# Kernel tuning notes

Measured on AMD Instinct MI355X. Metric: run time of the kernel, lower is better.

Reference implementation:

```python
import jax, jax.numpy as jnp
import numpy as np

B, N, D_IN, D_OUT = 2, 768, 64, 64
TEMP = 2.0
BN_EPS = 1e-5


def setup_inputs() -> dict:
    key = jax.random.key(0)
    ks = jax.random.split(key, 12)
    s_in = 1.0 / np.sqrt(D_IN)
    return {
        "x": jax.random.normal(ks[0], (B, N, D_IN), jnp.float32),
        # att_proj: Linear(in_dim, out_dim), stored as [in, out]
        "W_att": jax.random.uniform(ks[1], (D_IN, D_OUT), jnp.float32, -s_in, s_in),
        "b_att": jax.random.uniform(ks[2], (D_OUT,), jnp.float32, -s_in, s_in),
        # att_weight: [out_dim, 1] -> stored squeezed [out_dim]
        "a_w": jax.random.normal(ks[3], (D_OUT,), jnp.float32) * np.sqrt(2.0 / (D_OUT + 1)),
        "W_p": jax.random.uniform(ks[4], (D_IN, D_OUT), jnp.float32, -s_in, s_in),
        "b_p": jax.random.uniform(ks[5], (D_OUT,), jnp.float32, -s_in, s_in),
        "W_q": jax.random.uniform(ks[6], (D_IN, D_OUT), jnp.float32, -s_in, s_in),
        "b_q": jax.random.uniform(ks[7], (D_OUT,), jnp.float32, -s_in, s_in),
        # BatchNorm1d eval-mode params / running stats
        "gamma": jnp.ones((D_OUT,), jnp.float32),
        "beta": jnp.zeros((D_OUT,), jnp.float32),
        "r_mean": jax.random.normal(ks[8], (D_OUT,), jnp.float32) * 0.1,
        "r_var": jax.random.uniform(ks[9], (D_OUT,), jnp.float32, 0.5, 1.5),
    }


def reference(x, W_att, b_att, a_w, W_p, b_p, W_q, b_q, gamma, beta, r_mean, r_var):
    # pairwise node product: [B, N, N, D]
    pm = x[:, :, None, :] * x[:, None, :, :]
    # tanh(att_proj(pm)) @ att_weight -> scalar score per (i, j)
    h = jnp.tanh(jnp.einsum("bijd,do->bijo", pm, W_att) + b_att)
    scores = jnp.einsum("bijo,o->bij", h, a_w) / TEMP
    # softmax over dim=-2 of [B,N,N,1] == the j (second node) axis
    att = jax.nn.softmax(scores, axis=2)  # [B, N, N]
    # attention-weighted aggregation + skip projection
    agg = jnp.einsum("bij,bjd->bid", att, x)  # [B, N, D]
    y = agg @ W_p + b_p + x @ W_q + b_q  # [B, N, D_OUT]
    # BatchNorm1d (eval mode, running stats)
    y = (y - r_mean) * (gamma / jnp.sqrt(r_var + BN_EPS)) + beta
    return jax.nn.selu(y)
```

## Files before the change

kernel.cpp:

```cpp
#include <hip/hip_runtime.h>
#include <hip/hip_bf16.h>

constexpr int Bc = 2;
constexpr int Nc = 768;
constexpr int Dc = 64;

typedef __attribute__((ext_vector_type(8))) short short8;
typedef __attribute__((ext_vector_type(4))) short short4v;
typedef __attribute__((ext_vector_type(4))) float f32x4;

#define TWO_LOG2E 2.8853900817779268f

__device__ inline short fbf(float f) {
    __hip_bfloat16 h = __float2bfloat16(f);
    return *reinterpret_cast<short*>(&h);
}

__global__ __launch_bounds__(256)
void prep_kernel(const float* __restrict__ x, short* __restrict__ xb)
{
    const int idx = blockIdx.x * 256 + threadIdx.x;
    const float4 v = ((const float4*)x)[idx];
    short4v o;
    o[0] = fbf(v.x); o[1] = fbf(v.y); o[2] = fbf(v.z); o[3] = fbf(v.w);
    ((short4v*)xb)[idx] = o;
}

__global__ __launch_bounds__(256, 4)
void scores_kernel(const float* __restrict__ x,
                   const short* __restrict__ xbf,
                   const float* __restrict__ W_att,
                   const float* __restrict__ b_att,
                   const float* __restrict__ a_w,
                   float* __restrict__ sc)
{
    __shared__ short s_A[Dc * Dc];
    __shared__ float s_xi[Dc];

    const int blk = blockIdx.x;
    const int b   = blk & 1;
    const int i   = blk >> 1;
    const int tid  = threadIdx.x;
    const int lane = tid & 63;
    const int wid  = tid >> 6;

    const float* xb  = x   + (size_t)b * Nc * Dc;
    const short* xbb = xbf + (size_t)b * Nc * Dc;

    if (tid < Dc) s_xi[tid] = xb[i * Dc + tid];
    __syncthreads();

    {
        const int d0 = wid * 16;
        float m0[16];
#pragma unroll
        for (int dd = 0; dd < 16; ++dd)
            m0[dd] = s_xi[d0 + dd] * W_att[(d0 + dd) * Dc + lane];
#pragma unroll
        for (int c8 = 0; c8 < 2; ++c8) {
            short8 v;
#pragma unroll
            for (int e = 0; e < 8; ++e) v[e] = fbf(m0[c8 * 8 + e]);
            const int c    = wid * 2 + c8;
            const int phys = c ^ (lane & 7);
            *(short8*)(&s_A[lane * Dc + phys * 8]) = v;
        }
    }

    float tb2[16], aw[16];
#pragma unroll
    for (int mt = 0; mt < 4; ++mt)
#pragma unroll
        for (int r = 0; r < 4; ++r) {
            const int o = 16 * mt + 4 * (lane >> 4) + r;
            tb2[mt * 4 + r] = TWO_LOG2E * b_att[o];
            aw [mt * 4 + r] = a_w[o];
        }
    float sa = 0.f;
#pragma unroll
    for (int k = 0; k < 16; ++k) sa += aw[k];
    sa += __shfl_xor(sa, 16, 64);
    sa += __shfl_xor(sa, 32, 64);
    const float half_sum_aw = 0.5f * sa;
    __syncthreads();

    short8 afr[4][2];
#pragma unroll
    for (int mt = 0; mt < 4; ++mt)
#pragma unroll
        for (int kt = 0; kt < 2; ++kt) {
            const int o    = 16 * mt + (lane & 15);
            const int c    = (lane >> 4) + 4 * kt;
            const int phys = c ^ (o & 7);
            afr[mt][kt] = *(const short8*)(&s_A[o * Dc + phys * 8]);
        }

    float* srow = sc + ((size_t)b * Nc + i) * Nc;
    const int t0 = i >> 4;

    int t = t0 + wid;
    if (t < 48) {
        const short* p0 = xbb + (size_t)(16 * t + (lane & 15)) * Dc + (lane >> 4) * 8;
        short8 c0 = *(const short8*)p0;
        short8 c1 = *(const short8*)(p0 + 32);
        while (t < 48) {
            const int tn = t + 4;
            short8 n0, n1;
            if (tn < 48) {
                const short* p1 = xbb + (size_t)(16 * tn + (lane & 15)) * Dc + (lane >> 4) * 8;
                n0 = *(const short8*)p1;
                n1 = *(const short8*)(p1 + 32);
            }

            f32x4 ac[4];
#pragma unroll
            for (int mt = 0; mt < 4; ++mt) {
                ac[mt] = (f32x4){0.f, 0.f, 0.f, 0.f};
                ac[mt] = __builtin_amdgcn_mfma_f32_16x16x32_bf16(afr[mt][0], c0, ac[mt], 0, 0, 0);
                ac[mt] = __builtin_amdgcn_mfma_f32_16x16x32_bf16(afr[mt][1], c1, ac[mt], 0, 0, 0);
            }

            float p = 0.f;
#pragma unroll
            for (int mt = 0; mt < 4; ++mt)
#pragma unroll
                for (int r = 0; r < 4; ++r) {
                    const float m = fmaf(ac[mt][r], TWO_LOG2E, tb2[mt * 4 + r]);
                    const float e = __builtin_amdgcn_exp2f(m);
                    const float rc = __builtin_amdgcn_rcpf(e + 1.f);
                    p = fmaf(aw[mt * 4 + r], rc, p);
                }
            p += __shfl_xor(p, 16, 64);
            p += __shfl_xor(p, 32, 64);

            const int j = 16 * t + lane;
            if (lane < 16 && j >= i) srow[j] = half_sum_aw - p;
            c0 = n0; c1 = n1; t = tn;
        }
    }
}

__global__ __launch_bounds__(256, 4)
void finish_kernel(const float* __restrict__ x,
                   const float* __restrict__ sc,
                   const float* __restrict__ W_p,
                   const float* __restrict__ b_p,
                   const float* __restrict__ W_q,
                   const float* __restrict__ b_q,
                   const float* __restrict__ gamma,
                   const float* __restrict__ beta,
                   const float* __restrict__ r_mean,
                   const float* __restrict__ r_var,
                   float* __restrict__ out)
{
    __shared__ float s_score[Nc];
    __shared__ float s_xi[Dc];
    __shared__ float s_red[4][Dc];
    __shared__ float s_tmp[4];

    const int blk = blockIdx.x;
    const int b   = blk & 1;
    const int i   = blk >> 1;
    const int tid  = threadIdx.x;
    const int lane = tid & 63;
    const int wid  = tid >> 6;

    const float* xb = x + (size_t)b * Nc * Dc;
    if (tid < Dc) s_xi[tid] = xb[i * Dc + tid];

    const float* srow = sc + ((size_t)b * Nc + i) * Nc;
    for (int j = i + tid; j < Nc; j += 256) s_score[j] = srow[j];
    for (int j = tid; j < i; j += 256)      s_score[j] = sc[((size_t)b * Nc + j) * Nc + i];
    __syncthreads();

    float mx = -1e30f;
    for (int j = tid; j < Nc; j += 256) mx = fmaxf(mx, s_score[j]);
#pragma unroll
    for (int off = 32; off; off >>= 1)
        mx = fmaxf(mx, __shfl_xor(mx, off, 64));
    if (lane == 0) s_tmp[wid] = mx;
    __syncthreads();
    mx = fmaxf(fmaxf(s_tmp[0], s_tmp[1]), fmaxf(s_tmp[2], s_tmp[3]));
    __syncthreads();

    float sm = 0.f;
    for (int j = tid; j < Nc; j += 256) {
        const float e = __expf(s_score[j] - mx);
        s_score[j] = e;
        sm += e;
    }
#pragma unroll
    for (int off = 32; off; off >>= 1)
        sm += __shfl_xor(sm, off, 64);
    if (lane == 0) s_tmp[wid] = sm;
    __syncthreads();
    const float inv_sum = 1.f / (s_tmp[0] + s_tmp[1] + s_tmp[2] + s_tmp[3]);

    float aggp = 0.f;
    const int j0 = wid * (Nc / 4), j1 = j0 + Nc / 4;
    for (int j = j0; j < j1; ++j)
        aggp = fmaf(s_score[j], xb[j * Dc + lane], aggp);
    s_red[wid][lane] = aggp;
    __syncthreads();

    if (wid == 0)
        s_red[0][lane] = (s_red[0][lane] + s_red[1][lane] +
                          s_red[2][lane] + s_red[3][lane]) * inv_sum;
    __syncthreads();

    if (wid == 0) {
        float y = b_p[lane] + b_q[lane];
#pragma unroll 8
        for (int d = 0; d < Dc; ++d) {
            y = fmaf(s_red[0][d], W_p[d * Dc + lane], y);
            y = fmaf(s_xi[d],     W_q[d * Dc + lane], y);
        }
        const float inv_std = rsqrtf(r_var[lane] + 1e-5f);
        y = (y - r_mean[lane]) * (gamma[lane] * inv_std) + beta[lane];
        const float kScale = 1.0507009873554805f;
        const float kAlpha = 1.6732632423543772f;
        y = y > 0.f ? kScale * y : kScale * kAlpha * (__expf(y) - 1.f);
        out[((size_t)b * Nc + i) * Dc + lane] = y;
    }
}

__global__ __launch_bounds__(256, 4)
void mono_kernel(const float* __restrict__ x,
                 const float* __restrict__ W_att,
                 const float* __restrict__ b_att,
                 const float* __restrict__ a_w,
                 const float* __restrict__ W_p,
                 const float* __restrict__ b_p,
                 const float* __restrict__ W_q,
                 const float* __restrict__ b_q,
                 const float* __restrict__ gamma,
                 const float* __restrict__ beta,
                 const float* __restrict__ r_mean,
                 const float* __restrict__ r_var,
                 float* __restrict__ out)
{
    __shared__ short s_A[Dc * Dc];
    __shared__ float s_score[Nc];
    __shared__ float s_xi[Dc];
    __shared__ float s_red[4][Dc];
    __shared__ float s_tmp[4];

    const int bid = blockIdx.x;
    const int b   = bid / Nc;
    const int i   = bid - b * Nc;
    const int tid  = threadIdx.x;
    const int lane = tid & 63;
    const int wid  = tid >> 6;

    const float* xb = x + (size_t)b * Nc * Dc;
    if (tid < Dc) s_xi[tid] = xb[i * Dc + tid];
    __syncthreads();

    {
        const int d0 = wid * 16;
        float m0[16];
#pragma unroll
        for (int dd = 0; dd < 16; ++dd)
            m0[dd] = s_xi[d0 + dd] * W_att[(d0 + dd) * Dc + lane];
#pragma unroll
        for (int c8 = 0; c8 < 2; ++c8) {
            short8 v;
#pragma unroll
            for (int e = 0; e < 8; ++e) v[e] = fbf(m0[c8 * 8 + e]);
            const int c    = wid * 2 + c8;
            const int phys = c ^ (lane & 7);
            *(short8*)(&s_A[lane * Dc + phys * 8]) = v;
        }
    }

    float tb[16], aw[16];
#pragma unroll
    for (int mt = 0; mt < 4; ++mt)
#pragma unroll
        for (int r = 0; r < 4; ++r) {
            const int o = 16 * mt + 4 * (lane >> 4) + r;
            tb[mt * 4 + r] = 2.f * b_att[o];
            aw[mt * 4 + r] = a_w[o];
        }
    __syncthreads();

    short8 afr[4][2];
#pragma unroll
    for (int mt = 0; mt < 4; ++mt)
#pragma unroll
        for (int kt = 0; kt < 2; ++kt) {
            const int o    = 16 * mt + (lane & 15);
            const int c    = (lane >> 4) + 4 * kt;
            const int phys = c ^ (o & 7);
            afr[mt][kt] = *(const short8*)(&s_A[o * Dc + phys * 8]);
        }

    const int jbase = wid * 192;
    for (int t = 0; t < 12; ++t) {
        const int j0 = jbase + t * 16;
        const float* xr = xb + (size_t)(j0 + (lane & 15)) * Dc + (lane >> 4) * 8;
        const float4 v0 = *(const float4*)(xr);
        const float4 v1 = *(const float4*)(xr + 4);
        const float4 v2 = *(const float4*)(xr + 32);
        const float4 v3 = *(const float4*)(xr + 36);
        short8 bf0, bf1;
        bf0[0]=fbf(v0.x); bf0[1]=fbf(v0.y); bf0[2]=fbf(v0.z); bf0[3]=fbf(v0.w);
        bf0[4]=fbf(v1.x); bf0[5]=fbf(v1.y); bf0[6]=fbf(v1.z); bf0[7]=fbf(v1.w);
        bf1[0]=fbf(v2.x); bf1[1]=fbf(v2.y); bf1[2]=fbf(v2.z); bf1[3]=fbf(v2.w);
        bf1[4]=fbf(v3.x); bf1[5]=fbf(v3.y); bf1[6]=fbf(v3.z); bf1[7]=fbf(v3.w);

        f32x4 ac[4];
#pragma unroll
        for (int mt = 0; mt < 4; ++mt) {
            ac[mt] = (f32x4){0.f, 0.f, 0.f, 0.f};
            ac[mt] = __builtin_amdgcn_mfma_f32_16x16x32_bf16(afr[mt][0], bf0, ac[mt], 0, 0, 0);
            ac[mt] = __builtin_amdgcn_mfma_f32_16x16x32_bf16(afr[mt][1], bf1, ac[mt], 0, 0, 0);
        }

        float p = 0.f;
#pragma unroll
        for (int mt = 0; mt < 4; ++mt)
#pragma unroll
            for (int r = 0; r < 4; ++r) {
                const float e  = __expf(fmaf(ac[mt][r], 2.f, tb[mt * 4 + r]));
                const float th = 1.f - 2.f * __builtin_amdgcn_rcpf(e + 1.f);
                p = fmaf(th, aw[mt * 4 + r], p);
            }
        p += __shfl_xor(p, 16, 64);
        p += __shfl_xor(p, 32, 64);
        if (lane < 16) s_score[j0 + lane] = p * 0.5f;
    }
    __syncthreads();

    float mx = -1e30f;
    for (int j = tid; j < Nc; j += 256) mx = fmaxf(mx, s_score[j]);
#pragma unroll
    for (int off = 32; off; off >>= 1)
        mx = fmaxf(mx, __shfl_xor(mx, off, 64));
    if (lane == 0) s_tmp[wid] = mx;
    __syncthreads();
    mx = fmaxf(fmaxf(s_tmp[0], s_tmp[1]), fmaxf(s_tmp[2], s_tmp[3]));
    __syncthreads();

    float sm = 0.f;
    for (int j = tid; j < Nc; j += 256) {
        const float e = __expf(s_score[j] - mx);
        s_score[j] = e;
        sm += e;
    }
#pragma unroll
    for (int off = 32; off; off >>= 1)
        sm += __shfl_xor(sm, off, 64);
    if (lane == 0) s_tmp[wid] = sm;
    __syncthreads();
    const float inv_sum = 1.f / (s_tmp[0] + s_tmp[1] + s_tmp[2] + s_tmp[3]);

    float aggp = 0.f;
    const int j0 = wid * (Nc / 4), j1 = j0 + Nc / 4;
    for (int j = j0; j < j1; ++j)
        aggp = fmaf(s_score[j], xb[j * Dc + lane], aggp);
    s_red[wid][lane] = aggp;
    __syncthreads();

    if (wid == 0)
        s_red[0][lane] = (s_red[0][lane] + s_red[1][lane] +
                          s_red[2][lane] + s_red[3][lane]) * inv_sum;
    __syncthreads();

    if (wid == 0) {
        float y = b_p[lane] + b_q[lane];
#pragma unroll 8
        for (int d = 0; d < Dc; ++d) {
            y = fmaf(s_red[0][d], W_p[d * Dc + lane], y);
            y = fmaf(s_xi[d],     W_q[d * Dc + lane], y);
        }
        const float inv_std = rsqrtf(r_var[lane] + 1e-5f);
        y = (y - r_mean[lane]) * (gamma[lane] * inv_std) + beta[lane];
        const float kScale = 1.0507009873554805f;
        const float kAlpha = 1.6732632423543772f;
        y = y > 0.f ? kScale * y : kScale * kAlpha * (__expf(y) - 1.f);
        out[bid * Dc + lane] = y;
    }
}

extern "C" void kernel_launch(void* const* d_in, const int* in_sizes, int n_in,
                              void* d_out, int out_size, void* d_ws, size_t ws_size,
                              hipStream_t stream) {
    const float* x      = (const float*)d_in[0];
    const float* W_att  = (const float*)d_in[1];
    const float* b_att  = (const float*)d_in[2];
    const float* a_w    = (const float*)d_in[3];
    const float* W_p    = (const float*)d_in[4];
    const float* b_p    = (const float*)d_in[5];
    const float* W_q    = (const float*)d_in[6];
    const float* b_q    = (const float*)d_in[7];
    const float* gamma  = (const float*)d_in[8];
    const float* beta   = (const float*)d_in[9];
    const float* r_mean = (const float*)d_in[10];
    const float* r_var  = (const float*)d_in[11];
    float* out = (float*)d_out;

    constexpr size_t SC_OFF = 196608;
    constexpr size_t NEED   = SC_OFF + (size_t)Bc * Nc * Nc * 4;

    if (ws_size >= NEED) {
        short* x_bf   = (short*)d_ws;
        float* scores = (float*)((char*)d_ws + SC_OFF);
        prep_kernel  <<<dim3((Bc * Nc * Dc / 4) / 256), dim3(256), 0, stream>>>(x, x_bf);
        scores_kernel<<<dim3(Bc * Nc), dim3(256), 0, stream>>>(x, x_bf, W_att, b_att, a_w, scores);
        finish_kernel<<<dim3(Bc * Nc), dim3(256), 0, stream>>>(x, scores, W_p, b_p, W_q, b_q,
                                                               gamma, beta, r_mean, r_var, out);
    } else {
        mono_kernel<<<dim3(Bc * Nc), dim3(256), 0, stream>>>(
            x, W_att, b_att, a_w, W_p, b_p, W_q, b_q,
            gamma, beta, r_mean, r_var, out);
    }
}
```

Measured before the change: 43.24 us.

## Pair triangular rows for balanced score blocks and write symmetric scores

The scores kernel now pairs row i with row N-1-i so each pair covers a constant 49 tiles of the upper triangle, and splits those tiles across two blocks (25 and 24 tiles) to balance work per block. It also writes each score to both (i,j) and (j,i), so the finish kernel reads a contiguous row instead of a strided column gather. Scores are pre-scaled by log2(e) so softmax can use exp2 directly. The cost is extra scattered global writes for the mirrored entries, a second A-matrix tile in shared memory, and a change in grid mapping whose host launch is not shown.

New measurement: 44.15 us. +2.1%, slower.

```diff
diff --git a/kernel.cpp b/kernel.cpp
--- a/kernel.cpp
+++ b/kernel.cpp
@@ -4,12 +4,14 @@
 constexpr int Bc = 2;
 constexpr int Nc = 768;
 constexpr int Dc = 64;
+constexpr int NPAIR = Nc / 2;
 
 typedef __attribute__((ext_vector_type(8))) short short8;
 typedef __attribute__((ext_vector_type(4))) short short4v;
 typedef __attribute__((ext_vector_type(4))) float f32x4;
 
 #define TWO_LOG2E 2.8853900817779268f
+#define SCORE_SCALE 1.4426950408889634f
 
 __device__ inline short fbf(float f) {
     __hip_bfloat16 h = __float2bfloat16(f);
@@ -34,12 +36,18 @@
                    const float* __restrict__ a_w,
                    float* __restrict__ sc)
 {
-    __shared__ short s_A[Dc * Dc];
-    __shared__ float s_xi[Dc];
-
-    const int blk = blockIdx.x;
-    const int b   = blk & 1;
-    const int i   = blk >> 1;
+    __shared__ short s_A[2][Dc * Dc];
+    __shared__ float s_xr[2][Dc];
+
+    const int blk  = blockIdx.x;
+    const int pr   = blk >> 1;
+    const int half = blk & 1;
+    const int b    = pr / NPAIR;
+    const int q    = pr - b * NPAIR;
+    const int i1   = q;
+    const int i2   = Nc - 1 - q;
+    const int c1   = 48 - (i1 >> 4);
+
     const int tid  = threadIdx.x;
     const int lane = tid & 63;
     const int wid  = tid >> 6;
@@ -47,15 +55,19 @@
     const float* xb  = x   + (size_t)b * Nc * Dc;
     const short* xbb = xbf + (size_t)b * Nc * Dc;
 
-    if (tid < Dc) s_xi[tid] = xb[i * Dc + tid];
-    __syncthreads();
-
-    {
+    if (tid < 2 * Dc) {
+        const int r = tid >> 6;
+        s_xr[r][tid & 63] = xb[(r ? i2 : i1) * Dc + (tid & 63)];
+    }
+    __syncthreads();
+
+#pragma unroll
+    for (int rsel = 0; rsel < 2; ++rsel) {
         const int d0 = wid * 16;
         float m0[16];
 #pragma unroll
         for (int dd = 0; dd < 16; ++dd)
-            m0[dd] = s_xi[d0 + dd] * W_att[(d0 + dd) * Dc + lane];
+            m0[dd] = s_xr[rsel][d0 + dd] * W_att[(d0 + dd) * Dc + lane];
 #pragma unroll
         for (int c8 = 0; c8 < 2; ++c8) {
             short8 v;
@@ -63,7 +75,7 @@
             for (int e = 0; e < 8; ++e) v[e] = fbf(m0[c8 * 8 + e]);
             const int c    = wid * 2 + c8;
             const int phys = c ^ (lane & 7);
-            *(short8*)(&s_A[lane * Dc + phys * 8]) = v;
+            *(short8*)(&s_A[rsel][lane * Dc + phys * 8]) = v;
         }
     }
 
@@ -84,29 +96,42 @@
     const float half_sum_aw = 0.5f * sa;
     __syncthreads();
 
-    short8 afr[4][2];
-#pragma unroll
-    for (int mt = 0; mt < 4; ++mt)
-#pragma unroll
-        for (int kt = 0; kt < 2; ++kt) {
-            const int o    = 16 * mt + (lane & 15);
-            const int c    = (lane >> 4) + 4 * kt;
-            const int phys = c ^ (o & 7);
-            afr[mt][kt] = *(const short8*)(&s_A[o * Dc + phys * 8]);
-        }
-
-    float* srow = sc + ((size_t)b * Nc + i) * Nc;
-    const int t0 = i >> 4;
-
-    int t = t0 + wid;
-    if (t < 48) {
+    const int gend = 25 + half * 24;
+    int g = half * 25 + wid;
+
+    if (g < gend) {
+        auto tile_of = [&](int gg) {
+            return (gg < c1) ? (i1 >> 4) + gg : (i2 >> 4) + (gg - c1);
+        };
+
+        int t = tile_of(g);
         const short* p0 = xbb + (size_t)(16 * t + (lane & 15)) * Dc + (lane >> 4) * 8;
-        short8 c0 = *(const short8*)p0;
-        short8 c1 = *(const short8*)(p0 + 32);
-        while (t < 48) {
-            const int tn = t + 4;
+        short8 cb0 = *(const short8*)p0;
+        short8 cb1 = *(const short8*)(p0 + 32);
+
+        int cur = -1;
+        short8 afr[4][2];
+
+        while (g < gend) {
+            const int rsel = (g >= c1) ? 1 : 0;
+            if (rsel != cur) {
+#pragma unroll
+                for (int mt = 0; mt < 4; ++mt)
+#pragma unroll
+                    for (int kt = 0; kt < 2; ++kt) {
+                        const int o    = 16 * mt + (lane & 15);
+                        const int c    = (lane >> 4) + 4 * kt;
+                        const int phys = c ^ (o & 7);
+                        afr[mt][kt] = *(const short8*)(&s_A[rsel][o * Dc + phys * 8]);
+                    }
+                cur = rsel;
+            }
+
+            const int gn = g + 4;
+            int tn = 0;
             short8 n0, n1;
-            if (tn < 48) {
+            if (gn < gend) {
+                tn = tile_of(gn);
                 const short* p1 = xbb + (size_t)(16 * tn + (lane & 15)) * Dc + (lane >> 4) * 8;
                 n0 = *(const short8*)p1;
                 n1 = *(const short8*)(p1 + 32);
@@ -116,8 +141,8 @@
 #pragma unroll
             for (int mt = 0; mt < 4; ++mt) {
                 ac[mt] = (f32x4){0.f, 0.f, 0.f, 0.f};
-                ac[mt] = __builtin_amdgcn_mfma_f32_16x16x32_bf16(afr[mt][0], c0, ac[mt], 0, 0, 0);
-                ac[mt] = __builtin_amdgcn_mfma_f32_16x16x32_bf16(afr[mt][1], c1, ac[mt], 0, 0, 0);
+                ac[mt] = __builtin_amdgcn_mfma_f32_16x16x32_bf16(afr[mt][0], cb0, ac[mt], 0, 0, 0);
+                ac[mt] = __builtin_amdgcn_mfma_f32_16x16x32_bf16(afr[mt][1], cb1, ac[mt], 0, 0, 0);
             }
 
             float p = 0.f;
@@ -125,17 +150,22 @@
             for (int mt = 0; mt < 4; ++mt)
 #pragma unroll
                 for (int r = 0; r < 4; ++r) {
-                    const float m = fmaf(ac[mt][r], TWO_LOG2E, tb2[mt * 4 + r]);
-                    const float e = __builtin_amdgcn_exp2f(m);
+                    const float m  = fmaf(ac[mt][r], TWO_LOG2E, tb2[mt * 4 + r]);
+                    const float e  = __builtin_amdgcn_exp2f(m);
                     const float rc = __builtin_amdgcn_rcpf(e + 1.f);
                     p = fmaf(aw[mt * 4 + r], rc, p);
                 }
             p += __shfl_xor(p, 16, 64);
             p += __shfl_xor(p, 32, 64);
 
-            const int j = 16 * t + lane;
-            if (lane < 16 && j >= i) srow[j] = half_sum_aw - p;
-            c0 = n0; c1 = n1; t = tn;
+            const int ic = rsel ? i2 : i1;
+            const int j  = 16 * t + lane;
+            if (lane < 16) {
+                const float v = (half_sum_aw - p) * SCORE_SCALE;
+                if (j >= ic) sc[((size_t)b * Nc + ic) * Nc + j] = v;
+                if (j >  ic) sc[((size_t)b * Nc + j) * Nc + ic] = v;
+            }
+            cb0 = n0; cb1 = n1; g = gn; t = tn;
         }
     }
 }
@@ -169,8 +199,7 @@
     if (tid < Dc) s_xi[tid] = xb[i * Dc + tid];
 
     const float* srow = sc + ((size_t)b * Nc + i) * Nc;
-    for (int j = i + tid; j < Nc; j += 256) s_score[j] = srow[j];
-    for (int j = tid; j < i; j += 256)      s_score[j] = sc[((size_t)b * Nc + j) * Nc + i];
+    for (int j = tid; j < Nc; j += 256) s_score[j] = srow[j];
     __syncthreads();
 
     float mx = -1e30f;
@@ -185,7 +214,7 @@
 
     float sm = 0.f;
     for (int j = tid; j < Nc; j += 256) {
-        const float e = __expf(s_score[j] - mx);
+        const float e = __builtin_amdgcn_exp2f(s_score[j] - mx);
         s_score[j] = e;
         sm += e;
     }
```
